# Performance work log

Hardware: AMD Instinct MI355X
Metric: run time of the kernel (lower is better)

Reference implementation:

```python
import jax, jax.numpy as jnp
import numpy as np
from jax import lax

R_WIN = 1
WIN = 2 * R_WIN + 1        # 3
K = WIN * WIN              # 9
STRIDE = 4
LATENT = 128
N_LVL = 2


def _conv_relu(x, w, b):
    # x: (B*S, 3, H, W), w: (128, 3, 7, 7) -> (B*S, 128, H/4, W/4)
    y = lax.conv_general_dilated(x, w, (STRIDE, STRIDE), [(3, 3), (3, 3)],
                                 dimension_numbers=('NCHW', 'OIHW', 'NCHW'))
    return jax.nn.relu(y + b[None, :, None, None])


def _bilinear_sample(fmap, gx, gy):
    # fmap (B,C,H,W); gx,gy (B,P) in [-1,1]; align_corners=True, zeros padding
    B, C, H, W = fmap.shape
    ix = (gx + 1.0) * 0.5 * (W - 1)
    iy = (gy + 1.0) * 0.5 * (H - 1)
    x0 = jnp.floor(ix); y0 = jnp.floor(iy)
    x1 = x0 + 1.0;      y1 = y0 + 1.0
    wx1 = ix - x0; wx0 = 1.0 - wx1
    wy1 = iy - y0; wy0 = 1.0 - wy1

    fm_flat = fmap.reshape(B, C, H * W)

    def corner(xf, yf, wgt):
        valid = (xf >= 0) & (xf <= W - 1) & (yf >= 0) & (yf <= H - 1)
        xi = jnp.clip(xf, 0, W - 1).astype(jnp.int32)
        yi = jnp.clip(yf, 0, H - 1).astype(jnp.int32)
        idx = yi * W + xi                              # (B,P)
        g = jax.vmap(lambda fm, ii: fm[:, ii])(fm_flat, idx)  # (B,C,P)
        return g * (wgt * valid)[:, None, :]

    return (corner(x0, y0, wx0 * wy0) + corner(x1, y0, wx1 * wy0)
            + corner(x0, y1, wx0 * wy1) + corner(x1, y1, wx1 * wy1))


def _sample_features(fmap, pts):
    B, C, H, W = fmap.shape
    N = pts.shape[1]
    lin = jnp.linspace(-R_WIN, R_WIN, WIN)
    dy, dx = jnp.meshgrid(lin, lin, indexing='ij')
    off = jnp.stack([dx / (W - 1) * 2.0, dy / (H - 1) * 2.0], -1).reshape(-1, 2)  # (K,2)
    grid = (pts * 2.0 - 1.0)[:, :, None, :] + off[None, None]   # (B,N,K,2)
    grid = grid.reshape(B, N * K, 2)
    s = _bilinear_sample(fmap, grid[..., 0], grid[..., 1])       # (B,C,N*K)
    return s.reshape(B, C, N, WIN, WIN)


def _l2norm(x, axis):
    return x / jnp.maximum(jnp.linalg.norm(x, axis=axis, keepdims=True), 1e-12)


def _forward(queries, frames, conv_w, conv_b, w1, b1, wp, bp, wv, bv):
    B, S, C, H, W = frames.shape
    N = queries.shape[1]
    x = 2.0 * (frames / 255.0) - 1.0
    fm = _conv_relu(x.reshape(B * S, C, H, W), conv_w, conv_b)
    fm = fm.reshape(B, S, LATENT, H // STRIDE, W // STRIDE)

    pyr = [fm]
    for _ in range(N_LVL - 1):
        fm = lax.reduce_window(fm, 0.0, lax.add, (1, 1, 1, WIN, WIN),
                               (1, 1, 1, WIN, WIN), 'VALID') / float(WIN * WIN)
        pyr.append(fm)

    cur = queries                                   # pred_pos aliases queries in torch
    vis_acc = jnp.zeros((B, N), queries.dtype)
    for i in range(N_LVL):
        f5 = pyr[N_LVL - 1 - i]                     # (B,S,C,h,w) coarse -> fine
        feats = _sample_features(f5[:, 0], cur).reshape(B, LATENT, N, K)
        matches = _sample_features(f5[:, 1], cur).reshape(B, LATENT, N, K)
        fn = _l2norm(feats, 1)
        mn = _l2norm(matches, 1)
        corr = jnp.einsum('bcnh,bcnk->bnhk', fn, mn).reshape(B * N, K * K)
        h = jax.nn.relu(corr @ w1 + b1)
        pred = jax.nn.softmax(h @ wp + bp, axis=-1).reshape(B, N, WIN, WIN)
        vis = jax.nn.sigmoid(h @ wv + bv).reshape(B, N)
        hh, ww = f5.shape[3], f5.shape[4]
        dsx = jnp.linspace(-R_WIN / (ww - 1), R_WIN / (ww - 1), WIN)
        dsy = jnp.linspace(-R_WIN / (hh - 1), R_WIN / (hh - 1), WIN)
        d_x = pred.sum(-1) @ dsx                    # (B,N)
        d_y = pred.sum(-2) @ dsy                    # (B,N)
        cur = jnp.stack([cur[..., 0] + d_x, cur[..., 1] + d_y], -1)
        vis_acc = vis_acc + vis
    return cur, vis_acc / float(N_LVL)


def setup_inputs() -> dict:
    key = jax.random.key(0)
    ks = jax.random.split(key, 8)
    B, S, N, H, W = 2, 2, 8192, 384, 512
    return {
        'queries': jax.random.uniform(ks[0], (B, N, 2), jnp.float32),
        'frames': jax.random.uniform(ks[1], (B, S, 3, H, W), jnp.float32) * 255.0,
        'conv_w': jax.random.normal(ks[2], (128, 3, 7, 7), jnp.float32) * 0.02,
        'conv_b': jnp.zeros((128,), jnp.float32),
        'w1': jax.random.normal(ks[3], (81, 256), jnp.float32) * 0.05,
        'b1': jnp.zeros((256,), jnp.float32),
        'wp': jax.random.normal(ks[4], (256, 9), jnp.float32) * 0.05,
        'bp': jnp.zeros((9,), jnp.float32),
        'wv': jax.random.normal(ks[5], (256, 1), jnp.float32) * 0.05,
        'bv': jnp.zeros((1,), jnp.float32),
    }


def reference(queries, frames, conv_w, conv_b, w1, b1, wp, bp, wv, bv):
    return _forward(queries, frames, conv_w, conv_b, w1, b1, wp, bp, wv, bv)
```

## Files before the change

### kernel.cpp

```cpp
#include <hip/hip_runtime.h>
#include <math.h>

#define NQ 8192
#define NP 16384
#define H_IN 384
#define W_IN 512
#define HH0 96
#define WW0 128
#define HH1 32
#define WW1 42

__global__ void transpose_w_kernel(const float* __restrict__ w, float* __restrict__ wT) {
    int idx = blockIdx.x * 256 + threadIdx.x;
    if (idx < 147 * 128) {
        int tap = idx >> 7;
        int oc  = idx & 127;
        wT[idx] = w[oc * 147 + tap];
    }
}

__global__ __launch_bounds__(256, 4) void conv_kernel(
    const float* __restrict__ frames, const float* __restrict__ wT,
    const float* __restrict__ bias, float* __restrict__ out)
{
    __shared__ float lds[3 * 7 * 136];
    const int bs  = blockIdx.z;
    const int oh  = blockIdx.y;
    const int ow0 = blockIdx.x * 32;
    const int tid = threadIdx.x;

    for (int idx = tid; idx < 3 * 7 * 134; idx += 256) {
        int c   = idx / 938;
        int rem = idx - c * 938;
        int kh  = rem / 134;
        int col = rem - kh * 134;
        int gy  = oh * 4 - 3 + kh;
        int gx  = ow0 * 4 - 3 + col;
        float v = 0.0f;
        if (gy >= 0 && gy < H_IN && gx >= 0 && gx < W_IN) {
            float t = frames[((size_t)(bs * 3 + c) * H_IN + gy) * W_IN + gx];
            v = 2.0f * (t / 255.0f) - 1.0f;
        }
        lds[(c * 7 + kh) * 136 + col] = v;
    }
    __syncthreads();

    const int oc = tid & 63;
    const int g  = tid >> 6;
    float a0[8], a1[8];
#pragma unroll
    for (int p = 0; p < 8; ++p) { a0[p] = 0.0f; a1[p] = 0.0f; }

#pragma unroll
    for (int c = 0; c < 3; ++c) {
#pragma unroll
        for (int kh = 0; kh < 7; ++kh) {
            const float* row = lds + (c * 7 + kh) * 136 + g * 32;
            float4 r4[9];
#pragma unroll
            for (int j = 0; j < 9; ++j) r4[j] = *(const float4*)(row + j * 4);
            float w0[7], w1v[7];
#pragma unroll
            for (int kw = 0; kw < 7; ++kw) {
                int tap = (c * 7 + kh) * 7 + kw;
                w0[kw]  = wT[tap * 128 + oc];
                w1v[kw] = wT[tap * 128 + oc + 64];
            }
#pragma unroll
            for (int p = 0; p < 8; ++p) {
                const float4 A  = r4[p];
                const float4 Bv = r4[p + 1];
                float s0 = a0[p], s1 = a1[p];
                s0 = fmaf(A.x,  w0[0], s0);  s1 = fmaf(A.x,  w1v[0], s1);
                s0 = fmaf(A.y,  w0[1], s0);  s1 = fmaf(A.y,  w1v[1], s1);
                s0 = fmaf(A.z,  w0[2], s0);  s1 = fmaf(A.z,  w1v[2], s1);
                s0 = fmaf(A.w,  w0[3], s0);  s1 = fmaf(A.w,  w1v[3], s1);
                s0 = fmaf(Bv.x, w0[4], s0);  s1 = fmaf(Bv.x, w1v[4], s1);
                s0 = fmaf(Bv.y, w0[5], s0);  s1 = fmaf(Bv.y, w1v[5], s1);
                s0 = fmaf(Bv.z, w0[6], s0);  s1 = fmaf(Bv.z, w1v[6], s1);
                a0[p] = s0; a1[p] = s1;
            }
        }
    }

    const float b0  = bias[oc];
    const float b1b = bias[oc + 64];
#pragma unroll
    for (int p = 0; p < 8; ++p) {
        int ow = ow0 + g * 8 + p;
        size_t ob = ((size_t)(bs * HH0 + oh) * WW0 + ow) * 128;
        out[ob + oc]      = fmaxf(a0[p] + b0, 0.0f);
        out[ob + oc + 64] = fmaxf(a1[p] + b1b, 0.0f);
    }
}

__global__ void pool_kernel(const float* __restrict__ in, float* __restrict__ out) {
    int idx = blockIdx.x * 256 + threadIdx.x;
    if (idx >= 4 * HH1 * WW1 * 128) return;
    int c = idx & 127;
    int r = idx >> 7;
    int px = r % WW1; r /= WW1;
    int py = r % HH1;
    int bs = r / HH1;
    float s = 0.0f;
#pragma unroll
    for (int dy = 0; dy < 3; ++dy)
#pragma unroll
        for (int dx = 0; dx < 3; ++dx)
            s += in[(((size_t)bs * HH0 + py * 3 + dy) * WW0 + px * 3 + dx) * 128 + c];
    out[idx] = s / 9.0f;
}

__global__ __launch_bounds__(512) void sample_kernel(
    const float* __restrict__ fm, int hh, int ww,
    const float* __restrict__ cur_in, float* __restrict__ corr_out)
{
    __shared__ float smem[4 * 2400];
    const int tid  = threadIdx.x;
    const int wvi  = tid >> 6;
    const int lane = tid & 63;
    const int ps   = wvi >> 1;
    const int mp   = wvi & 1;
    const int p    = blockIdx.x * 4 + ps;
    const int b    = p >> 13;

    float* fl    = smem + ps * 2400;
    float* ml    = fl + 1188;
    float* inv_s = fl + 2376;

    const float2 pxy = *(const float2*)(cur_in + (size_t)p * 2);
    const float wwm1 = (float)(ww - 1);
    const float hhm1 = (float)(hh - 1);
    const float ix = ((pxy.x * 2.0f - 1.0f) + 1.0f) * 0.5f * wwm1;
    const float iy = ((pxy.y * 2.0f - 1.0f) + 1.0f) * 0.5f * hhm1;
    const float x0 = floorf(ix), y0 = floorf(iy);
    const float fx1 = ix - x0, fx0 = 1.0f - fx1;
    const float fy1 = iy - y0, fy0 = 1.0f - fy1;

    int   cx[4], cy[4];
    float vx[4], vy[4];
#pragma unroll
    for (int j = 0; j < 4; ++j) {
        float xc = x0 + (float)(j - 1);
        vx[j] = (xc >= 0.0f && xc <= wwm1) ? 1.0f : 0.0f;
        cx[j] = (int)fminf(fmaxf(xc, 0.0f), wwm1);
        float yc = y0 + (float)(j - 1);
        vy[j] = (yc >= 0.0f && yc <= hhm1) ? 1.0f : 0.0f;
        cy[j] = (int)fminf(fmaxf(yc, 0.0f), hhm1);
    }
    float cwx[6], cwy[6];
#pragma unroll
    for (int t = 0; t < 3; ++t) {
        cwx[t * 2 + 0] = fx0 * vx[t]; cwx[t * 2 + 1] = fx1 * vx[t + 1];
        cwy[t * 2 + 0] = fy0 * vy[t]; cwy[t * 2 + 1] = fy1 * vy[t + 1];
    }

    {
        const float2* src = (const float2*)fm + (size_t)(b * 2 + mp) * hh * ww * 64;
        float* dst = mp ? ml : fl;
        float2 P[4][4];
#pragma unroll
        for (int j = 0; j < 4; ++j)
#pragma unroll
            for (int i = 0; i < 4; ++i)
                P[j][i] = src[(cy[j] * ww + cx[i]) * 64 + lane];
#pragma unroll
        for (int ky = 0; ky < 3; ++ky)
#pragma unroll
            for (int kx = 0; kx < 3; ++kx) {
                float wA = cwy[ky * 2 + 0] * cwx[kx * 2 + 0];
                float wB = cwy[ky * 2 + 0] * cwx[kx * 2 + 1];
                float wC = cwy[ky * 2 + 1] * cwx[kx * 2 + 0];
                float wD = cwy[ky * 2 + 1] * cwx[kx * 2 + 1];
                float sx = wA * P[ky][kx].x;
                sx = fmaf(wB, P[ky][kx + 1].x, sx);
                sx = fmaf(wC, P[ky + 1][kx].x, sx);
                sx = fmaf(wD, P[ky + 1][kx + 1].x, sx);
                float sy = wA * P[ky][kx].y;
                sy = fmaf(wB, P[ky][kx + 1].y, sy);
                sy = fmaf(wC, P[ky + 1][kx].y, sy);
                sy = fmaf(wD, P[ky + 1][kx + 1].y, sy);
                *(float2*)(dst + (ky * 3 + kx) * 132 + 2 * lane) = make_float2(sx, sy);
            }
    }
    __syncthreads();

    const int e = mp * 64 + lane;
    float s = 0.0f;
    {
        const float *rA, *rB;
        if (e < 81)      { rA = fl + (e / 9) * 132; rB = ml + (e % 9) * 132; }
        else if (e < 90) { rA = fl + (e - 81) * 132; rB = rA; }
        else             { int em = e - 90; if (em > 8) em = 8;
                           rA = ml + em * 132; rB = rA; }
#pragma unroll
        for (int c = 0; c < 128; c += 4) {
            float4 a  = *(const float4*)(rA + c);
            float4 bb = *(const float4*)(rB + c);
            s += a.x * bb.x; s += a.y * bb.y; s += a.z * bb.z; s += a.w * bb.w;
        }
    }
    if (e >= 81 && e < 90)      inv_s[e - 81]     = 1.0f / fmaxf(sqrtf(s), 1e-12f);
    else if (e >= 90 && e < 99) inv_s[e - 90 + 9] = 1.0f / fmaxf(sqrtf(s), 1e-12f);
    __syncthreads();

    if (e < 81)
        corr_out[(size_t)p * 81 + e] = s * inv_s[e / 9] * inv_s[9 + e % 9];
}

__global__ __launch_bounds__(512) void mlp_kernel(
    const float* __restrict__ corr, const float* __restrict__ cur_in,
    const float* __restrict__ w1, const float* __restrict__ b1,
    const float* __restrict__ wp, const float* __restrict__ bp,
    const float* __restrict__ wvw, const float* __restrict__ bvv,
    int hh, int ww,
    float* __restrict__ cur_out,
    const float* __restrict__ vis_in, float* __restrict__ vis_out,
    int is_last)
{
    __shared__ float w1L[81 * 256];
    __shared__ float corrL[81 * 68];
    __shared__ float wpL[256 * 9];
    __shared__ float wvL[256];
    __shared__ float b1L[256];
    const int tid   = threadIdx.x;
    const int jg    = tid & 31;
    const int pg    = tid >> 5;
    const int j0    = jg * 8;
    const int pbase = blockIdx.x * 64;

    {
        const float4* src = (const float4*)w1;
        float4*       dst = (float4*)w1L;
        for (int idx = tid; idx < 5184; idx += 512) dst[idx] = src[idx];
    }
    for (int idx = tid; idx < 64 * 81; idx += 512) {
        int pt = idx / 81, i = idx - pt * 81;
        corrL[i * 68 + pt] = corr[(size_t)pbase * 81 + idx];
    }
    for (int idx = tid; idx < 2304; idx += 512) wpL[idx] = wp[idx];
    if (tid < 256) { wvL[tid] = wvw[tid]; b1L[tid] = b1[tid]; }
    __syncthreads();

    float h[4][8];
#pragma unroll
    for (int j = 0; j < 8; ++j) {
        const float bj = b1L[j0 + j];
#pragma unroll
        for (int p = 0; p < 4; ++p) h[p][j] = bj;
    }

    const float* wlp = w1L + j0;
    const float* cvp = corrL + pg * 4;
#pragma unroll 3
    for (int i = 0; i < 81; ++i) {
        const float4 wa = *(const float4*)(wlp + i * 256);
        const float4 wb = *(const float4*)(wlp + i * 256 + 4);
        const float4 cv = *(const float4*)(cvp + i * 68);
        const float c4[4] = {cv.x, cv.y, cv.z, cv.w};
#pragma unroll
        for (int p = 0; p < 4; ++p) {
            h[p][0] = fmaf(c4[p], wa.x, h[p][0]);
            h[p][1] = fmaf(c4[p], wa.y, h[p][1]);
            h[p][2] = fmaf(c4[p], wa.z, h[p][2]);
            h[p][3] = fmaf(c4[p], wa.w, h[p][3]);
            h[p][4] = fmaf(c4[p], wb.x, h[p][4]);
            h[p][5] = fmaf(c4[p], wb.y, h[p][5]);
            h[p][6] = fmaf(c4[p], wb.z, h[p][6]);
            h[p][7] = fmaf(c4[p], wb.w, h[p][7]);
        }
    }

    float pl[4][10];
#pragma unroll
    for (int p = 0; p < 4; ++p)
#pragma unroll
        for (int o = 0; o < 10; ++o) pl[p][o] = 0.0f;
#pragma unroll
    for (int j = 0; j < 8; ++j) {
        const float* wr = wpL + (j0 + j) * 9;
        const float wvv = wvL[j0 + j];
#pragma unroll
        for (int p = 0; p < 4; ++p) {
            const float hv = fmaxf(h[p][j], 0.0f);
#pragma unroll
            for (int o = 0; o < 9; ++o) pl[p][o] = fmaf(hv, wr[o], pl[p][o]);
            pl[p][9] = fmaf(hv, wvv, pl[p][9]);
        }
    }
#pragma unroll
    for (int p = 0; p < 4; ++p)
#pragma unroll
        for (int o = 0; o < 10; ++o) {
            pl[p][o] += __shfl_xor(pl[p][o], 1);
            pl[p][o] += __shfl_xor(pl[p][o], 2);
            pl[p][o] += __shfl_xor(pl[p][o], 4);
            pl[p][o] += __shfl_xor(pl[p][o], 8);
            pl[p][o] += __shfl_xor(pl[p][o], 16);
        }

    if (jg == 0) {
        const float wwm1 = (float)(ww - 1);
        const float hhm1 = (float)(hh - 1);
        const float ax = 1.0f / wwm1;
        const float ay = 1.0f / hhm1;
#pragma unroll
        for (int t = 0; t < 4; ++t) {
            const float* fo = pl[t];
            const int p = pbase + pg * 4 + t;
            float lg[9];
#pragma unroll
            for (int o = 0; o < 9; ++o) lg[o] = fo[o] + bp[o];
            float mx = lg[0];
#pragma unroll
            for (int o = 1; o < 9; ++o) mx = fmaxf(mx, lg[o]);
            float ex[9], sum = 0.0f;
#pragma unroll
            for (int o = 0; o < 9; ++o) { ex[o] = expf(lg[o] - mx); sum += ex[o]; }
#pragma unroll
            for (int o = 0; o < 9; ++o) ex[o] = ex[o] / sum;

            const float vis = 1.0f / (1.0f + expf(-(fo[9] + bvv[0])));

            const float r0 = ex[0] + ex[1] + ex[2];
            const float r2 = ex[6] + ex[7] + ex[8];
            const float c0 = ex[0] + ex[3] + ex[6];
            const float c2 = ex[2] + ex[5] + ex[8];
            const float dx = r0 * (-ax) + r2 * ax;
            const float dy = c0 * (-ay) + c2 * ay;

            const float2 pq = *(const float2*)(cur_in + (size_t)p * 2);
            *(float2*)(cur_out + (size_t)p * 2) = make_float2(pq.x + dx, pq.y + dy);
            vis_out[p] = is_last ? (vis_in[p] + vis) * 0.5f : vis;
        }
    }
}

extern "C" void kernel_launch(void* const* d_in, const int* in_sizes, int n_in,
                              void* d_out, int out_size, void* d_ws, size_t ws_size,
                              hipStream_t stream) {
    (void)in_sizes; (void)n_in; (void)out_size; (void)ws_size;
    const float* queries = (const float*)d_in[0];
    const float* frames  = (const float*)d_in[1];
    const float* conv_w  = (const float*)d_in[2];
    const float* conv_b  = (const float*)d_in[3];
    const float* w1      = (const float*)d_in[4];
    const float* b1      = (const float*)d_in[5];
    const float* wp      = (const float*)d_in[6];
    const float* bp      = (const float*)d_in[7];
    const float* wvw     = (const float*)d_in[8];
    const float* bvv     = (const float*)d_in[9];
    float* out = (float*)d_out;

    float* ws     = (float*)d_ws;
    float* fm0    = ws;
    float* fm1    = fm0 + 6291456;
    float* wT     = fm1 + 688128;
    float* cur_ws = wT + 18816;
    float* vis_ws = cur_ws + 32768;
    float* corrws = vis_ws + 16384;

    transpose_w_kernel<<<74, 256, 0, stream>>>(conv_w, wT);
    conv_kernel<<<dim3(4, HH0, 4), 256, 0, stream>>>(frames, wT, conv_b, fm0);
    pool_kernel<<<2688, 256, 0, stream>>>(fm0, fm1);

    sample_kernel<<<4096, 512, 0, stream>>>(fm1, HH1, WW1, queries, corrws);
    mlp_kernel<<<256, 512, 0, stream>>>(corrws, queries, w1, b1, wp, bp, wvw, bvv,
                                        HH1, WW1, cur_ws, nullptr, vis_ws, 0);
    sample_kernel<<<4096, 512, 0, stream>>>(fm0, HH0, WW0, cur_ws, corrws);
    mlp_kernel<<<256, 512, 0, stream>>>(corrws, cur_ws, w1, b1, wp, bp, wvw, bvv,
                                        HH0, WW0, out, vis_ws, out + 32768, 1);
}
```

Before: 231.7 us.

## Fuse correlation sampling and MLP head into one per-level kernel

Merges the sample and MLP kernels so each block computes the 81-entry correlation for four points, keeps it in shared memory, and runs the MLP, softmax and visibility head in the same block. This removes the global round trip of the correlation buffer and two kernel launches. In exchange, each block now reads w1, wp and wv straight from global memory (4096 blocks each pulling the full weights through cache) rather than staging them once in shared memory per 64 points. The first-layer work is split across lanes with shuffle and shared-memory reductions, which adds sync overhead.

```diff
diff --git a/kernel.cpp b/kernel.cpp
--- a/kernel.cpp
+++ b/kernel.cpp
@@ -111,11 +111,19 @@
     out[idx] = s / 9.0f;
 }
 
-__global__ __launch_bounds__(512) void sample_kernel(
+__global__ __launch_bounds__(512, 6) void level_fused_kernel(
     const float* __restrict__ fm, int hh, int ww,
-    const float* __restrict__ cur_in, float* __restrict__ corr_out)
+    const float* __restrict__ cur_in,
+    const float* __restrict__ w1, const float* __restrict__ b1,
+    const float* __restrict__ wp, const float* __restrict__ bp,
+    const float* __restrict__ wvw, const float* __restrict__ bvv,
+    float* __restrict__ cur_out,
+    const float* __restrict__ vis_in, float* __restrict__ vis_out,
+    int is_last)
 {
     __shared__ float smem[4 * 2400];
+    __shared__ float cls[4 * 84];
+    __shared__ float red[8 * 4 * 10];
     const int tid  = threadIdx.x;
     const int wvi  = tid >> 6;
     const int lane = tid & 63;
@@ -128,34 +136,34 @@
     float* ml    = fl + 1188;
     float* inv_s = fl + 2376;
 
-    const float2 pxy = *(const float2*)(cur_in + (size_t)p * 2);
-    const float wwm1 = (float)(ww - 1);
-    const float hhm1 = (float)(hh - 1);
-    const float ix = ((pxy.x * 2.0f - 1.0f) + 1.0f) * 0.5f * wwm1;
-    const float iy = ((pxy.y * 2.0f - 1.0f) + 1.0f) * 0.5f * hhm1;
-    const float x0 = floorf(ix), y0 = floorf(iy);
-    const float fx1 = ix - x0, fx0 = 1.0f - fx1;
-    const float fy1 = iy - y0, fy0 = 1.0f - fy1;
-
-    int   cx[4], cy[4];
-    float vx[4], vy[4];
-#pragma unroll
-    for (int j = 0; j < 4; ++j) {
-        float xc = x0 + (float)(j - 1);
-        vx[j] = (xc >= 0.0f && xc <= wwm1) ? 1.0f : 0.0f;
-        cx[j] = (int)fminf(fmaxf(xc, 0.0f), wwm1);
-        float yc = y0 + (float)(j - 1);
-        vy[j] = (yc >= 0.0f && yc <= hhm1) ? 1.0f : 0.0f;
-        cy[j] = (int)fminf(fmaxf(yc, 0.0f), hhm1);
-    }
-    float cwx[6], cwy[6];
-#pragma unroll
-    for (int t = 0; t < 3; ++t) {
-        cwx[t * 2 + 0] = fx0 * vx[t]; cwx[t * 2 + 1] = fx1 * vx[t + 1];
-        cwy[t * 2 + 0] = fy0 * vy[t]; cwy[t * 2 + 1] = fy1 * vy[t + 1];
-    }
-
     {
+        const float2 pxy = *(const float2*)(cur_in + (size_t)p * 2);
+        const float wwm1 = (float)(ww - 1);
+        const float hhm1 = (float)(hh - 1);
+        const float ix = ((pxy.x * 2.0f - 1.0f) + 1.0f) * 0.5f * wwm1;
+        const float iy = ((pxy.y * 2.0f - 1.0f) + 1.0f) * 0.5f * hhm1;
+        const float x0 = floorf(ix), y0 = floorf(iy);
+        const float fx1 = ix - x0, fx0 = 1.0f - fx1;
+        const float fy1 = iy - y0, fy0 = 1.0f - fy1;
+
+        int   cx[4], cy[4];
+        float vx[4], vy[4];
+#pragma unroll
+        for (int j = 0; j < 4; ++j) {
+            float xc = x0 + (float)(j - 1);
+            vx[j] = (xc >= 0.0f && xc <= wwm1) ? 1.0f : 0.0f;
+            cx[j] = (int)fminf(fmaxf(xc, 0.0f), wwm1);
+            float yc = y0 + (float)(j - 1);
+            vy[j] = (yc >= 0.0f && yc <= hhm1) ? 1.0f : 0.0f;
+            cy[j] = (int)fminf(fmaxf(yc, 0.0f), hhm1);
+        }
+        float cwx[6], cwy[6];
+#pragma unroll
+        for (int t = 0; t < 3; ++t) {
+            cwx[t * 2 + 0] = fx0 * vx[t]; cwx[t * 2 + 1] = fx1 * vx[t + 1];
+            cwy[t * 2 + 0] = fy0 * vy[t]; cwy[t * 2 + 1] = fy1 * vy[t + 1];
+        }
+
         const float2* src = (const float2*)fm + (size_t)(b * 2 + mp) * hh * ww * 64;
         float* dst = mp ? ml : fl;
         float2 P[4][4];
@@ -185,154 +193,130 @@
     }
     __syncthreads();
 
-    const int e = mp * 64 + lane;
-    float s = 0.0f;
     {
-        const float *rA, *rB;
-        if (e < 81)      { rA = fl + (e / 9) * 132; rB = ml + (e % 9) * 132; }
-        else if (e < 90) { rA = fl + (e - 81) * 132; rB = rA; }
-        else             { int em = e - 90; if (em > 8) em = 8;
-                           rA = ml + em * 132; rB = rA; }
-#pragma unroll
-        for (int c = 0; c < 128; c += 4) {
-            float4 a  = *(const float4*)(rA + c);
-            float4 bb = *(const float4*)(rB + c);
-            s += a.x * bb.x; s += a.y * bb.y; s += a.z * bb.z; s += a.w * bb.w;
-        }
-    }
-    if (e >= 81 && e < 90)      inv_s[e - 81]     = 1.0f / fmaxf(sqrtf(s), 1e-12f);
-    else if (e >= 90 && e < 99) inv_s[e - 90 + 9] = 1.0f / fmaxf(sqrtf(s), 1e-12f);
+        const int e = mp * 64 + lane;
+        float s = 0.0f;
+        {
+            const float *rA, *rB;
+            if (e < 81)      { rA = fl + (e / 9) * 132; rB = ml + (e % 9) * 132; }
+            else if (e < 90) { rA = fl + (e - 81) * 132; rB = rA; }
+            else             { int em = e - 90; if (em > 8) em = 8;
+                               rA = ml + em * 132; rB = rA; }
+#pragma unroll
+            for (int c = 0; c < 128; c += 4) {
+                float4 a  = *(const float4*)(rA + c);
+                float4 bb = *(const float4*)(rB + c);
+                s += a.x * bb.x; s += a.y * bb.y; s += a.z * bb.z; s += a.w * bb.w;
+            }
+        }
+        if (e >= 81 && e < 90)      inv_s[e - 81]     = 1.0f / fmaxf(sqrtf(s), 1e-12f);
+        else if (e >= 90 && e < 99) inv_s[e - 90 + 9] = 1.0f / fmaxf(sqrtf(s), 1e-12f);
+        __syncthreads();
+        if (e < 81)
+            cls[ps * 84 + e] = s * inv_s[e / 9] * inv_s[9 + e % 9];
+    }
     __syncthreads();
 
-    if (e < 81)
-        corr_out[(size_t)p * 81 + e] = s * inv_s[e / 9] * inv_s[9 + e % 9];
-}
-
-__global__ __launch_bounds__(512) void mlp_kernel(
-    const float* __restrict__ corr, const float* __restrict__ cur_in,
-    const float* __restrict__ w1, const float* __restrict__ b1,
-    const float* __restrict__ wp, const float* __restrict__ bp,
-    const float* __restrict__ wvw, const float* __restrict__ bvv,
-    int hh, int ww,
-    float* __restrict__ cur_out,
-    const float* __restrict__ vis_in, float* __restrict__ vis_out,
-    int is_last)
-{
-    __shared__ float w1L[81 * 256];
-    __shared__ float corrL[81 * 68];
-    __shared__ float wpL[256 * 9];
-    __shared__ float wvL[256];
-    __shared__ float b1L[256];
-    const int tid   = threadIdx.x;
-    const int jg    = tid & 31;
-    const int pg    = tid >> 5;
-    const int j0    = jg * 8;
-    const int pbase = blockIdx.x * 64;
+    const int kc  = lane & 3;
+    const int pt  = (lane >> 2) & 3;
+    const int jgl = lane >> 4;
+    const int jg  = wvi * 4 + jgl;
+    const int j0  = jg * 8;
+
+    float h[8];
+#pragma unroll
+    for (int j = 0; j < 8; ++j) h[j] = 0.0f;
 
     {
-        const float4* src = (const float4*)w1;
-        float4*       dst = (float4*)w1L;
-        for (int idx = tid; idx < 5184; idx += 512) dst[idx] = src[idx];
-    }
-    for (int idx = tid; idx < 64 * 81; idx += 512) {
-        int pt = idx / 81, i = idx - pt * 81;
-        corrL[i * 68 + pt] = corr[(size_t)pbase * 81 + idx];
-    }
-    for (int idx = tid; idx < 2304; idx += 512) wpL[idx] = wp[idx];
-    if (tid < 256) { wvL[tid] = wvw[tid]; b1L[tid] = b1[tid]; }
+        const float* wbase = w1 + j0;
+        const float* crow  = cls + pt * 84;
+        const int i0   = kc * 20;
+        const int icnt = (kc == 3) ? 21 : 20;
+#pragma unroll 4
+        for (int ii = 0; ii < icnt; ++ii) {
+            const int i = i0 + ii;
+            const float4 wa = *(const float4*)(wbase + i * 256);
+            const float4 wb = *(const float4*)(wbase + i * 256 + 4);
+            const float cv = crow[i];
+            h[0] = fmaf(cv, wa.x, h[0]); h[1] = fmaf(cv, wa.y, h[1]);
+            h[2] = fmaf(cv, wa.z, h[2]); h[3] = fmaf(cv, wa.w, h[3]);
+            h[4] = fmaf(cv, wb.x, h[4]); h[5] = fmaf(cv, wb.y, h[5]);
+            h[6] = fmaf(cv, wb.z, h[6]); h[7] = fmaf(cv, wb.w, h[7]);
+        }
+    }
+#pragma unroll
+    for (int j = 0; j < 8; ++j) {
+        h[j] += __shfl_xor(h[j], 1);
+        h[j] += __shfl_xor(h[j], 2);
+    }
+
+    float b1v[8];
+    {
+        const float4* bp4 = (const float4*)(b1 + j0);
+        const float4 ba = bp4[0], bb = bp4[1];
+        b1v[0] = ba.x; b1v[1] = ba.y; b1v[2] = ba.z; b1v[3] = ba.w;
+        b1v[4] = bb.x; b1v[5] = bb.y; b1v[6] = bb.z; b1v[7] = bb.w;
+    }
+    float pl[10];
+#pragma unroll
+    for (int o = 0; o < 10; ++o) pl[o] = 0.0f;
+#pragma unroll
+    for (int j = 0; j < 8; ++j) {
+        const float hv = fmaxf(h[j] + b1v[j], 0.0f);
+        const float* wr = wp + (j0 + j) * 9;
+#pragma unroll
+        for (int o = 0; o < 9; ++o) pl[o] = fmaf(hv, wr[o], pl[o]);
+        pl[9] = fmaf(hv, wvw[j0 + j], pl[9]);
+    }
+#pragma unroll
+    for (int o = 0; o < 10; ++o) {
+        pl[o] += __shfl_xor(pl[o], 16);
+        pl[o] += __shfl_xor(pl[o], 32);
+    }
+    if (lane == pt * 4) {
+#pragma unroll
+        for (int o = 0; o < 10; ++o) red[(wvi * 4 + pt) * 10 + o] = pl[o];
+    }
     __syncthreads();
 
-    float h[4][8];
-#pragma unroll
-    for (int j = 0; j < 8; ++j) {
-        const float bj = b1L[j0 + j];
-#pragma unroll
-        for (int p = 0; p < 4; ++p) h[p][j] = bj;
-    }
-
-    const float* wlp = w1L + j0;
-    const float* cvp = corrL + pg * 4;
-#pragma unroll 3
-    for (int i = 0; i < 81; ++i) {
-        const float4 wa = *(const float4*)(wlp + i * 256);
-        const float4 wb = *(const float4*)(wlp + i * 256 + 4);
-        const float4 cv = *(const float4*)(cvp + i * 68);
-        const float c4[4] = {cv.x, cv.y, cv.z, cv.w};
-#pragma unroll
-        for (int p = 0; p < 4; ++p) {
-            h[p][0] = fmaf(c4[p], wa.x, h[p][0]);
-            h[p][1] = fmaf(c4[p], wa.y, h[p][1]);
-            h[p][2] = fmaf(c4[p], wa.z, h[p][2]);
-            h[p][3] = fmaf(c4[p], wa.w, h[p][3]);
-            h[p][4] = fmaf(c4[p], wb.x, h[p][4]);
-            h[p][5] = fmaf(c4[p], wb.y, h[p][5]);
-            h[p][6] = fmaf(c4[p], wb.z, h[p][6]);
-            h[p][7] = fmaf(c4[p], wb.w, h[p][7]);
-        }
-    }
-
-    float pl[4][10];
-#pragma unroll
-    for (int p = 0; p < 4; ++p)
-#pragma unroll
-        for (int o = 0; o < 10; ++o) pl[p][o] = 0.0f;
-#pragma unroll
-    for (int j = 0; j < 8; ++j) {
-        const float* wr = wpL + (j0 + j) * 9;
-        const float wvv = wvL[j0 + j];
-#pragma unroll
-        for (int p = 0; p < 4; ++p) {
-            const float hv = fmaxf(h[p][j], 0.0f);
-#pragma unroll
-            for (int o = 0; o < 9; ++o) pl[p][o] = fmaf(hv, wr[o], pl[p][o]);
-            pl[p][9] = fmaf(hv, wvv, pl[p][9]);
-        }
-    }
-#pragma unroll
-    for (int p = 0; p < 4; ++p)
+    if (tid < 4) {
+        const int pw = blockIdx.x * 4 + tid;
+        float fo[10];
 #pragma unroll
         for (int o = 0; o < 10; ++o) {
-            pl[p][o] += __shfl_xor(pl[p][o], 1);
-            pl[p][o] += __shfl_xor(pl[p][o], 2);
-            pl[p][o] += __shfl_xor(pl[p][o], 4);
-            pl[p][o] += __shfl_xor(pl[p][o], 8);
-            pl[p][o] += __shfl_xor(pl[p][o], 16);
-        }
-
-    if (jg == 0) {
+            float v = 0.0f;
+#pragma unroll
+            for (int w = 0; w < 8; ++w) v += red[(w * 4 + tid) * 10 + o];
+            fo[o] = v;
+        }
+        float lg[9];
+#pragma unroll
+        for (int o = 0; o < 9; ++o) lg[o] = fo[o] + bp[o];
+        float mx = lg[0];
+#pragma unroll
+        for (int o = 1; o < 9; ++o) mx = fmaxf(mx, lg[o]);
+        float ex[9], sum = 0.0f;
+#pragma unroll
+        for (int o = 0; o < 9; ++o) { ex[o] = expf(lg[o] - mx); sum += ex[o]; }
+#pragma unroll
+        for (int o = 0; o < 9; ++o) ex[o] = ex[o] / sum;
+
+        const float vis = 1.0f / (1.0f + expf(-(fo[9] + bvv[0])));
+
         const float wwm1 = (float)(ww - 1);
         const float hhm1 = (float)(hh - 1);
         const float ax = 1.0f / wwm1;
         const float ay = 1.0f / hhm1;
-#pragma unroll
-        for (int t = 0; t < 4; ++t) {
-            const float* fo = pl[t];
-            const int p = pbase + pg * 4 + t;
-            float lg[9];
-#pragma unroll
-            for (int o = 0; o < 9; ++o) lg[o] = fo[o] + bp[o];
-            float mx = lg[0];
-#pragma unroll
-            for (int o = 1; o < 9; ++o) mx = fmaxf(mx, lg[o]);
-            float ex[9], sum = 0.0f;
-#pragma unroll
-            for (int o = 0; o < 9; ++o) { ex[o] = expf(lg[o] - mx); sum += ex[o]; }
-#pragma unroll
-            for (int o = 0; o < 9; ++o) ex[o] = ex[o] / sum;
-
-            const float vis = 1.0f / (1.0f + expf(-(fo[9] + bvv[0])));
-
-            const float r0 = ex[0] + ex[1] + ex[2];
-            const float r2 = ex[6] + ex[7] + ex[8];
-            const float c0 = ex[0] + ex[3] + ex[6];
-            const float c2 = ex[2] + ex[5] + ex[8];
-            const float dx = r0 * (-ax) + r2 * ax;
-            const float dy = c0 * (-ay) + c2 * ay;
-
-            const float2 pq = *(const float2*)(cur_in + (size_t)p * 2);
-            *(float2*)(cur_out + (size_t)p * 2) = make_float2(pq.x + dx, pq.y + dy);
-            vis_out[p] = is_last ? (vis_in[p] + vis) * 0.5f : vis;
-        }
+        const float r0 = ex[0] + ex[1] + ex[2];
+        const float r2 = ex[6] + ex[7] + ex[8];
+        const float c0 = ex[0] + ex[3] + ex[6];
+        const float c2 = ex[2] + ex[5] + ex[8];
+        const float dx = r0 * (-ax) + r2 * ax;
+        const float dy = c0 * (-ay) + c2 * ay;
+
+        const float2 pq = *(const float2*)(cur_in + (size_t)pw * 2);
+        *(float2*)(cur_out + (size_t)pw * 2) = make_float2(pq.x + dx, pq.y + dy);
+        vis_out[pw] = is_last ? (vis_in[pw] + vis) * 0.5f : vis;
     }
 }
 
@@ -358,16 +342,15 @@
     float* wT     = fm1 + 688128;
     float* cur_ws = wT + 18816;
     float* vis_ws = cur_ws + 32768;
-    float* corrws = vis_ws + 16384;
 
     transpose_w_kernel<<<74, 256, 0, stream>>>(conv_w, wT);
     conv_kernel<<<dim3(4, HH0, 4), 256, 0, stream>>>(frames, wT, conv_b, fm0);
     pool_kernel<<<2688, 256, 0, stream>>>(fm0, fm1);
 
-    sample_kernel<<<4096, 512, 0, stream>>>(fm1, HH1, WW1, queries, corrws);
-    mlp_kernel<<<256, 512, 0, stream>>>(corrws, queries, w1, b1, wp, bp, wvw, bvv,
-                                        HH1, WW1, cur_ws, nullptr, vis_ws, 0);
-    sample_kernel<<<4096, 512, 0, stream>>>(fm0, HH0, WW0, cur_ws, corrws);
-    mlp_kernel<<<256, 512, 0, stream>>>(corrws, cur_ws, w1, b1, wp, bp, wvw, bvv,
-                                        HH0, WW0, out, vis_ws, out + 32768, 1);
-}
+    level_fused_kernel<<<4096, 512, 0, stream>>>(fm1, HH1, WW1, queries,
+                                                 w1, b1, wp, bp, wvw, bvv,
+                                                 cur_ws, nullptr, vis_ws, 0);
+    level_fused_kernel<<<4096, 512, 0, stream>>>(fm0, HH0, WW0, cur_ws,
+                                                 w1, b1, wp, bp, wvw, bvv,
+                                                 out, vis_ws, out + 32768, 1);
+}
```

After: 480.8 us. +107.5%, slower.

## Restructure MLP kernel to one point per lane with wave-uniform weight broadcast

Applied to the files above, without the earlier changes.

Each wavefront now owns 64 hidden units and each lane one point, so weight reads from shared memory are wave-uniform broadcasts and each lane keeps 64 hidden accumulators in registers. The correlation tile is stored point-major with padding, and the cross-wave reduction of the 10 head outputs goes through shared memory instead of shuffle trees. Block size drops from 512 to 256 threads. This aims to cut LDS traffic and shuffle overhead, but it raises register pressure and leaves only 4 waves per block, with a single wave doing the softmax epilogue.

```diff
diff --git a/kernel.cpp b/kernel.cpp
--- a/kernel.cpp
+++ b/kernel.cpp
@@ -208,7 +208,7 @@
         corr_out[(size_t)p * 81 + e] = s * inv_s[e / 9] * inv_s[9 + e % 9];
 }
 
-__global__ __launch_bounds__(512) void mlp_kernel(
+__global__ __launch_bounds__(256, 1) void mlp_kernel(
     const float* __restrict__ corr, const float* __restrict__ cur_in,
     const float* __restrict__ w1, const float* __restrict__ b1,
     const float* __restrict__ wp, const float* __restrict__ bp,
@@ -219,120 +219,102 @@
     int is_last)
 {
     __shared__ float w1L[81 * 256];
-    __shared__ float corrL[81 * 68];
+    __shared__ float clsL[64 * 85];
     __shared__ float wpL[256 * 9];
     __shared__ float wvL[256];
     __shared__ float b1L[256];
+    __shared__ float red[256 * 10];
     const int tid   = threadIdx.x;
-    const int jg    = tid & 31;
-    const int pg    = tid >> 5;
-    const int j0    = jg * 8;
+    const int wvi   = tid >> 6;
+    const int lane  = tid & 63;
+    const int j0    = wvi * 64;
     const int pbase = blockIdx.x * 64;
 
     {
         const float4* src = (const float4*)w1;
         float4*       dst = (float4*)w1L;
-        for (int idx = tid; idx < 5184; idx += 512) dst[idx] = src[idx];
-    }
-    for (int idx = tid; idx < 64 * 81; idx += 512) {
+        for (int idx = tid; idx < 5184; idx += 256) dst[idx] = src[idx];
+    }
+    for (int idx = tid; idx < 64 * 81; idx += 256) {
         int pt = idx / 81, i = idx - pt * 81;
-        corrL[i * 68 + pt] = corr[(size_t)pbase * 81 + idx];
-    }
-    for (int idx = tid; idx < 2304; idx += 512) wpL[idx] = wp[idx];
+        clsL[pt * 85 + i] = corr[(size_t)pbase * 81 + idx];
+    }
+    for (int idx = tid; idx < 2304; idx += 256) wpL[idx] = wp[idx];
     if (tid < 256) { wvL[tid] = wvw[tid]; b1L[tid] = b1[tid]; }
     __syncthreads();
 
-    float h[4][8];
-#pragma unroll
-    for (int j = 0; j < 8; ++j) {
-        const float bj = b1L[j0 + j];
-#pragma unroll
-        for (int p = 0; p < 4; ++p) h[p][j] = bj;
-    }
-
-    const float* wlp = w1L + j0;
-    const float* cvp = corrL + pg * 4;
-#pragma unroll 3
+    float h[64];
+#pragma unroll
+    for (int jj = 0; jj < 64; ++jj) h[jj] = 0.0f;
+
+    const float* crow = clsL + lane * 85;
     for (int i = 0; i < 81; ++i) {
-        const float4 wa = *(const float4*)(wlp + i * 256);
-        const float4 wb = *(const float4*)(wlp + i * 256 + 4);
-        const float4 cv = *(const float4*)(cvp + i * 68);
-        const float c4[4] = {cv.x, cv.y, cv.z, cv.w};
-#pragma unroll
-        for (int p = 0; p < 4; ++p) {
-            h[p][0] = fmaf(c4[p], wa.x, h[p][0]);
-            h[p][1] = fmaf(c4[p], wa.y, h[p][1]);
-            h[p][2] = fmaf(c4[p], wa.z, h[p][2]);
-            h[p][3] = fmaf(c4[p], wa.w, h[p][3]);
-            h[p][4] = fmaf(c4[p], wb.x, h[p][4]);
-            h[p][5] = fmaf(c4[p], wb.y, h[p][5]);
-            h[p][6] = fmaf(c4[p], wb.z, h[p][6]);
-            h[p][7] = fmaf(c4[p], wb.w, h[p][7]);
-        }
-    }
-
-    float pl[4][10];
-#pragma unroll
-    for (int p = 0; p < 4; ++p)
-#pragma unroll
-        for (int o = 0; o < 10; ++o) pl[p][o] = 0.0f;
-#pragma unroll
-    for (int j = 0; j < 8; ++j) {
-        const float* wr = wpL + (j0 + j) * 9;
-        const float wvv = wvL[j0 + j];
-#pragma unroll
-        for (int p = 0; p < 4; ++p) {
-            const float hv = fmaxf(h[p][j], 0.0f);
-#pragma unroll
-            for (int o = 0; o < 9; ++o) pl[p][o] = fmaf(hv, wr[o], pl[p][o]);
-            pl[p][9] = fmaf(hv, wvv, pl[p][9]);
-        }
-    }
-#pragma unroll
-    for (int p = 0; p < 4; ++p)
+        const float cv = crow[i];
+        const float4* wrow = (const float4*)(w1L + i * 256 + j0);
+#pragma unroll
+        for (int q = 0; q < 16; ++q) {
+            const float4 w4 = wrow[q];
+            h[q * 4 + 0] = fmaf(cv, w4.x, h[q * 4 + 0]);
+            h[q * 4 + 1] = fmaf(cv, w4.y, h[q * 4 + 1]);
+            h[q * 4 + 2] = fmaf(cv, w4.z, h[q * 4 + 2]);
+            h[q * 4 + 3] = fmaf(cv, w4.w, h[q * 4 + 3]);
+        }
+    }
+
+    float pl[10];
+#pragma unroll
+    for (int o = 0; o < 10; ++o) pl[o] = 0.0f;
+#pragma unroll
+    for (int jj = 0; jj < 64; ++jj) {
+        const float hv = fmaxf(h[jj] + b1L[j0 + jj], 0.0f);
+        const float* wr = wpL + (j0 + jj) * 9;
+#pragma unroll
+        for (int o = 0; o < 9; ++o) pl[o] = fmaf(hv, wr[o], pl[o]);
+        pl[9] = fmaf(hv, wvL[j0 + jj], pl[9]);
+    }
+#pragma unroll
+    for (int o = 0; o < 10; ++o) red[(wvi * 64 + lane) * 10 + o] = pl[o];
+    __syncthreads();
+
+    if (wvi == 0) {
+        const int p = pbase + lane;
+        float fo[10];
 #pragma unroll
         for (int o = 0; o < 10; ++o) {
-            pl[p][o] += __shfl_xor(pl[p][o], 1);
-            pl[p][o] += __shfl_xor(pl[p][o], 2);
-            pl[p][o] += __shfl_xor(pl[p][o], 4);
-            pl[p][o] += __shfl_xor(pl[p][o], 8);
-            pl[p][o] += __shfl_xor(pl[p][o], 16);
-        }
-
-    if (jg == 0) {
+            float v = red[lane * 10 + o];
+            v += red[(64 + lane) * 10 + o];
+            v += red[(128 + lane) * 10 + o];
+            v += red[(192 + lane) * 10 + o];
+            fo[o] = v;
+        }
+        float lg[9];
+#pragma unroll
+        for (int o = 0; o < 9; ++o) lg[o] = fo[o] + bp[o];
+        float mx = lg[0];
+#pragma unroll
+        for (int o = 1; o < 9; ++o) mx = fmaxf(mx, lg[o]);
+        float ex[9], sum = 0.0f;
+#pragma unroll
+        for (int o = 0; o < 9; ++o) { ex[o] = expf(lg[o] - mx); sum += ex[o]; }
+#pragma unroll
+        for (int o = 0; o < 9; ++o) ex[o] = ex[o] / sum;
+
+        const float vis = 1.0f / (1.0f + expf(-(fo[9] + bvv[0])));
+
         const float wwm1 = (float)(ww - 1);
         const float hhm1 = (float)(hh - 1);
         const float ax = 1.0f / wwm1;
         const float ay = 1.0f / hhm1;
-#pragma unroll
-        for (int t = 0; t < 4; ++t) {
-            const float* fo = pl[t];
-            const int p = pbase + pg * 4 + t;
-            float lg[9];
-#pragma unroll
-            for (int o = 0; o < 9; ++o) lg[o] = fo[o] + bp[o];
-            float mx = lg[0];
-#pragma unroll
-            for (int o = 1; o < 9; ++o) mx = fmaxf(mx, lg[o]);
-            float ex[9], sum = 0.0f;
-#pragma unroll
-            for (int o = 0; o < 9; ++o) { ex[o] = expf(lg[o] - mx); sum += ex[o]; }
-#pragma unroll
-            for (int o = 0; o < 9; ++o) ex[o] = ex[o] / sum;
-
-            const float vis = 1.0f / (1.0f + expf(-(fo[9] + bvv[0])));
-
-            const float r0 = ex[0] + ex[1] + ex[2];
-            const float r2 = ex[6] + ex[7] + ex[8];
-            const float c0 = ex[0] + ex[3] + ex[6];
-            const float c2 = ex[2] + ex[5] + ex[8];
-            const float dx = r0 * (-ax) + r2 * ax;
-            const float dy = c0 * (-ay) + c2 * ay;
-
-            const float2 pq = *(const float2*)(cur_in + (size_t)p * 2);
-            *(float2*)(cur_out + (size_t)p * 2) = make_float2(pq.x + dx, pq.y + dy);
-            vis_out[p] = is_last ? (vis_in[p] + vis) * 0.5f : vis;
-        }
+        const float r0 = ex[0] + ex[1] + ex[2];
+        const float r2 = ex[6] + ex[7] + ex[8];
+        const float c0 = ex[0] + ex[3] + ex[6];
+        const float c2 = ex[2] + ex[5] + ex[8];
+        const float dx = r0 * (-ax) + r2 * ax;
+        const float dy = c0 * (-ay) + c2 * ay;
+
+        const float2 pq = *(const float2*)(cur_in + (size_t)p * 2);
+        *(float2*)(cur_out + (size_t)p * 2) = make_float2(pq.x + dx, pq.y + dy);
+        vis_out[p] = is_last ? (vis_in[p] + vis) * 0.5f : vis;
     }
 }
 
@@ -365,9 +347,9 @@
     pool_kernel<<<2688, 256, 0, stream>>>(fm0, fm1);
 
     sample_kernel<<<4096, 512, 0, stream>>>(fm1, HH1, WW1, queries, corrws);
-    mlp_kernel<<<256, 512, 0, stream>>>(corrws, queries, w1, b1, wp, bp, wvw, bvv,
+    mlp_kernel<<<256, 256, 0, stream>>>(corrws, queries, w1, b1, wp, bp, wvw, bvv,
                                         HH1, WW1, cur_ws, nullptr, vis_ws, 0);
     sample_kernel<<<4096, 512, 0, stream>>>(fm0, HH0, WW0, cur_ws, corrws);
-    mlp_kernel<<<256, 512, 0, stream>>>(corrws, cur_ws, w1, b1, wp, bp, wvw, bvv,
+    mlp_kernel<<<256, 256, 0, stream>>>(corrws, cur_ws, w1, b1, wp, bp, wvw, bvv,
                                         HH0, WW0, out, vis_ws, out + 32768, 1);
 }
```

New measurement: 236.8 us. +2.2%, slower.
